# Performance work log

Hardware: AMD Instinct MI355X
Metric: run time of the kernel (lower is better)

Reference implementation:

```python
import jax, jax.numpy as jnp
import numpy as np

B, C_IN, H, W = 8, 64, 256, 256
C_OUT, K, N_KERNELS = 128, 3, 8
PAD = K // 2


def setup_inputs() -> dict:
    key = jax.random.key(0)
    k1, k2, k3, k4 = jax.random.split(key, 4)
    x = jax.random.normal(k1, (B, C_IN, H, W), dtype=jnp.float32)
    kernel_bank = jax.random.normal(k2, (N_KERNELS, C_OUT, C_IN, K, K), dtype=jnp.float32)
    # nn.Linear(in_channels, num_kernels): weight (N, C_IN), bias (N,)
    lim = 1.0 / np.sqrt(C_IN)
    attn_w = jax.random.uniform(k3, (N_KERNELS, C_IN), minval=-lim, maxval=lim, dtype=jnp.float32)
    attn_b = jax.random.uniform(k4, (N_KERNELS,), minval=-lim, maxval=lim, dtype=jnp.float32)
    return {"x": x, "kernel_bank": kernel_bank, "attn_w": attn_w, "attn_b": attn_b}


def _per_sample_conv(xi, wi):
    # xi: (C_IN, H, W), wi: (C_OUT, C_IN, K, K)
    out = jax.lax.conv_general_dilated(
        xi[None], wi, window_strides=(1, 1), padding=[(PAD, PAD), (PAD, PAD)],
        dimension_numbers=("NCHW", "OIHW", "NCHW"))
    return out[0]


def reference(x, kernel_bank, attn_w, attn_b):
    pooled = jnp.mean(x, axis=(2, 3))                      # (B, C_IN)
    logits = pooled @ attn_w.T + attn_b                     # (B, N)
    attn = jax.nn.softmax(logits, axis=1)                   # (B, N)
    # Fused kernel mix: avoid (B, N, O, I, K, K) intermediate
    mixed = jnp.einsum("bn,noihw->boihw", attn, kernel_bank)  # (B, O, I, K, K)
    return jax.vmap(_per_sample_conv)(x, mixed)             # (B, O, H, W)
```

## Files before the change

### kernel.cpp

```cpp
#include <hip/hip_runtime.h>
#include <hip/hip_bf16.h>

#define B_     8
#define C_IN   64
#define C_OUT  128
#define HW     256
#define NK     8
#define KS     3

typedef __attribute__((ext_vector_type(8))) short bf16x8;
typedef __attribute__((ext_vector_type(4))) float f32x4;

__device__ inline unsigned short f2bf(float f) {
    union { float f; unsigned int u; } a; a.f = f;
    unsigned int u = a.u;
    u += 0x7fffu + ((u >> 16) & 1u);
    return (unsigned short)(u >> 16);
}

__global__ __launch_bounds__(256) void pool_kernel(const float* __restrict__ x,
                                                   float* __restrict__ pooled) {
    const int plane = blockIdx.x;
    const float4* p = (const float4*)(x + (size_t)plane * HW * HW);
    float s = 0.f;
    for (int idx = threadIdx.x; idx < (HW * HW) / 4; idx += 256) {
        float4 v = p[idx];
        s += v.x + v.y + v.z + v.w;
    }
    #pragma unroll
    for (int off = 32; off > 0; off >>= 1) s += __shfl_down(s, off, 64);
    __shared__ float ls[4];
    const int lane = threadIdx.x & 63, wv = threadIdx.x >> 6;
    if (lane == 0) ls[wv] = s;
    __syncthreads();
    if (threadIdx.x == 0) {
        float t = ls[0] + ls[1] + ls[2] + ls[3];
        pooled[plane] = t * (1.0f / (HW * HW));
    }
}

__global__ void attn_kernel(const float* __restrict__ pooled,
                            const float* __restrict__ attn_w,
                            const float* __restrict__ attn_b,
                            float* __restrict__ attn) {
    const int t = threadIdx.x;
    const int b = t >> 3, n = t & 7;
    float s = attn_b[n];
    #pragma unroll 8
    for (int c = 0; c < C_IN; c++) s += pooled[b * C_IN + c] * attn_w[n * C_IN + c];
    __shared__ float logits[B_ * NK];
    logits[t] = s;
    __syncthreads();
    float m = -1e30f;
    #pragma unroll
    for (int j = 0; j < NK; j++) m = fmaxf(m, logits[b * NK + j]);
    float denom = 0.f;
    #pragma unroll
    for (int j = 0; j < NK; j++) denom += expf(logits[b * NK + j] - m);
    attn[t] = expf(s - m) / denom;
}

__global__ __launch_bounds__(256) void mix_kernel(const float* __restrict__ bank,
                                                  const float* __restrict__ attn,
                                                  unsigned short* __restrict__ Wt2) {
    const int PER_B = C_OUT * C_IN * KS * KS;
    int idx = blockIdx.x * 256 + threadIdx.x;
    int b = idx / PER_B;
    int r = idx % PER_B;
    float s = 0.f;
    #pragma unroll
    for (int n = 0; n < NK; n++) s += attn[b * NK + n] * bank[(size_t)n * PER_B + r];
    int kw = r % 3;
    int t1 = r / 3;
    int kh = t1 % 3;
    int t2 = t1 / 3;
    int i = t2 & 63;
    int o = t2 >> 6;
    size_t off = (((size_t)((b * 3 + kh) * 3 + kw) * 2 + (i >> 5)) * 128 + o) * 32 + (i & 31);
    Wt2[off] = f2bf(s);
}

__global__ __launch_bounds__(256) void conv_mfma(const float* __restrict__ x,
                                                 const short* __restrict__ Wt2,
                                                 float* __restrict__ out) {
    const int w0 = blockIdx.x * 128;
    const int h  = blockIdx.y;
    const int b  = blockIdx.z;

    const int t    = threadIdx.x;
    const int lane = t & 63;
    const int wid  = t >> 6;
    const int wm   = (wid & 1) * 64;
    const int wn   = (wid >> 1) * 64;
    const int l15  = lane & 15;
    const int quad = lane >> 4;

    __shared__ short sxs[130 * 72];

    f32x4 acc[4][4];
    #pragma unroll
    for (int mt = 0; mt < 4; mt++)
        #pragma unroll
        for (int nt = 0; nt < 4; nt++)
            acc[mt][nt] = (f32x4){0.f, 0.f, 0.f, 0.f};

    for (int kh = 0; kh < 3; kh++) {
        __syncthreads();
        const int hr = h + kh - 1;
        const bool rv = (hr >= 0) && (hr < HW);
        {
            const int wl = t & 127;
            const int w  = w0 + wl - 1;
            const bool wvalid = rv && (w >= 0) && (w < HW);
            #pragma unroll
            for (int it = 0; it < 16; it++) {
                const int ip = it * 2 + (t >> 7);
                float v0 = 0.f, v1 = 0.f;
                if (wvalid) {
                    const float* px = x + (((size_t)(b * C_IN + 2 * ip) * HW + hr) * HW + w);
                    v0 = px[0];
                    v1 = px[HW * HW];
                }
                ushort2 u;
                u.x = f2bf(v0);
                u.y = f2bf(v1);
                *(ushort2*)&sxs[wl * 72 + 2 * ip] = u;
            }
            if (t < 128) {
                const int i2  = t >> 1;
                const int wl2 = 128 + (t & 1);
                const int w2  = w0 + wl2 - 1;
                unsigned short uv = 0;
                if (rv && w2 < HW)
                    uv = f2bf(x[((size_t)(b * C_IN + i2) * HW + hr) * HW + w2]);
                ((unsigned short*)sxs)[wl2 * 72 + i2] = uv;
            }
        }
        __syncthreads();

        const short* wbase = Wt2 + (size_t)((b * 3 + kh) * 3) * 2 * 4096;
        #pragma unroll
        for (int kw = 0; kw < 3; kw++) {
            #pragma unroll
            for (int ic = 0; ic < 2; ic++) {
                const short* Ap = wbase + (size_t)(kw * 2 + ic) * 4096
                                + (wm + l15) * 32 + quad * 8;
                bf16x8 a0 = *(const bf16x8*)(Ap);
                bf16x8 a1 = *(const bf16x8*)(Ap + 512);
                bf16x8 a2 = *(const bf16x8*)(Ap + 1024);
                bf16x8 a3 = *(const bf16x8*)(Ap + 1536);
                const short* Bp = sxs + (wn + l15 + kw) * 72 + ic * 32 + quad * 8;
                bf16x8 b0 = *(const bf16x8*)(Bp);
                bf16x8 b1 = *(const bf16x8*)(Bp + 16 * 72);
                bf16x8 b2 = *(const bf16x8*)(Bp + 32 * 72);
                bf16x8 b3 = *(const bf16x8*)(Bp + 48 * 72);
                acc[0][0] = __builtin_amdgcn_mfma_f32_16x16x32_bf16(a0, b0, acc[0][0], 0, 0, 0);
                acc[0][1] = __builtin_amdgcn_mfma_f32_16x16x32_bf16(a0, b1, acc[0][1], 0, 0, 0);
                acc[0][2] = __builtin_amdgcn_mfma_f32_16x16x32_bf16(a0, b2, acc[0][2], 0, 0, 0);
                acc[0][3] = __builtin_amdgcn_mfma_f32_16x16x32_bf16(a0, b3, acc[0][3], 0, 0, 0);
                acc[1][0] = __builtin_amdgcn_mfma_f32_16x16x32_bf16(a1, b0, acc[1][0], 0, 0, 0);
                acc[1][1] = __builtin_amdgcn_mfma_f32_16x16x32_bf16(a1, b1, acc[1][1], 0, 0, 0);
                acc[1][2] = __builtin_amdgcn_mfma_f32_16x16x32_bf16(a1, b2, acc[1][2], 0, 0, 0);
                acc[1][3] = __builtin_amdgcn_mfma_f32_16x16x32_bf16(a1, b3, acc[1][3], 0, 0, 0);
                acc[2][0] = __builtin_amdgcn_mfma_f32_16x16x32_bf16(a2, b0, acc[2][0], 0, 0, 0);
                acc[2][1] = __builtin_amdgcn_mfma_f32_16x16x32_bf16(a2, b1, acc[2][1], 0, 0, 0);
                acc[2][2] = __builtin_amdgcn_mfma_f32_16x16x32_bf16(a2, b2, acc[2][2], 0, 0, 0);
                acc[2][3] = __builtin_amdgcn_mfma_f32_16x16x32_bf16(a2, b3, acc[2][3], 0, 0, 0);
                acc[3][0] = __builtin_amdgcn_mfma_f32_16x16x32_bf16(a3, b0, acc[3][0], 0, 0, 0);
                acc[3][1] = __builtin_amdgcn_mfma_f32_16x16x32_bf16(a3, b1, acc[3][1], 0, 0, 0);
                acc[3][2] = __builtin_amdgcn_mfma_f32_16x16x32_bf16(a3, b2, acc[3][2], 0, 0, 0);
                acc[3][3] = __builtin_amdgcn_mfma_f32_16x16x32_bf16(a3, b3, acc[3][3], 0, 0, 0);
            }
        }
    }

    #pragma unroll
    for (int mt = 0; mt < 4; mt++) {
        const int o = wm + mt * 16 + quad * 4;
        #pragma unroll
        for (int nt = 0; nt < 4; nt++) {
            const int w = w0 + wn + nt * 16 + l15;
            float* op = out + (((size_t)(b * C_OUT + o) * HW + h) * HW + w);
            #pragma unroll
            for (int r = 0; r < 4; r++) op[(size_t)r * HW * HW] = acc[mt][nt][r];
        }
    }
}

extern "C" void kernel_launch(void* const* d_in, const int* in_sizes, int n_in,
                              void* d_out, int out_size, void* d_ws, size_t ws_size,
                              hipStream_t stream) {
    const float* x      = (const float*)d_in[0];
    const float* bank   = (const float*)d_in[1];
    const float* attn_w = (const float*)d_in[2];
    const float* attn_b = (const float*)d_in[3];
    float* out = (float*)d_out;

    unsigned short* Wt2 = (unsigned short*)d_ws;
    float* pooled = (float*)((char*)d_ws + 589824 * sizeof(short));
    float* attn   = pooled + B_ * C_IN;

    pool_kernel<<<B_ * C_IN, 256, 0, stream>>>(x, pooled);
    attn_kernel<<<1, 64, 0, stream>>>(pooled, attn_w, attn_b, attn);
    mix_kernel<<<(B_ * C_OUT * C_IN * KS * KS) / 256, 256, 0, stream>>>(bank, attn, Wt2);
    conv_mfma<<<dim3(2, HW, B_), 256, 0, stream>>>(x, (const short*)Wt2, out);
}
```

Baseline: 547.1 us.

## Pre-transpose input to padded bf16 NHWC and pipeline row slabs via LDS DMA

Adds a prepass that converts x into a zero-padded, channel-innermost, XOR-swizzled bf16 layout and computes the pooled means alongside it with atomics, replacing the separate pool pass. The conv kernel now processes 8 output rows per block and streams input rows through a 4-slot LDS ring with global_load_lds, prefetching three rows ahead, so each input row is reused across its three kh taps instead of being reloaded and reconverted from fp32. The cost is an extra pass that writes about 68 MB of bf16 plus a larger workspace requirement. If the workspace is too small, the code falls back to the old path.

```diff
diff --git a/kernel.cpp b/kernel.cpp
--- a/kernel.cpp
+++ b/kernel.cpp
@@ -10,6 +10,7 @@
 
 typedef __attribute__((ext_vector_type(8))) short bf16x8;
 typedef __attribute__((ext_vector_type(4))) float f32x4;
+typedef __attribute__((ext_vector_type(4))) unsigned int u32x4;
 
 __device__ inline unsigned short f2bf(float f) {
     union { float f; unsigned int u; } a; a.f = f;
@@ -17,25 +18,68 @@
     u += 0x7fffu + ((u >> 16) & 1u);
     return (unsigned short)(u >> 16);
 }
-
-__global__ __launch_bounds__(256) void pool_kernel(const float* __restrict__ x,
-                                                   float* __restrict__ pooled) {
-    const int plane = blockIdx.x;
-    const float4* p = (const float4*)(x + (size_t)plane * HW * HW);
+__device__ inline float bf2f(unsigned short u) {
+    union { float f; unsigned int u; } a; a.u = ((unsigned int)u) << 16; return a.f;
+}
+
+#define XT_PLANE  (258 * 64)
+#define SLAB_B    16640
+
+__global__ __launch_bounds__(256) void prepass_kernel(const float* __restrict__ x,
+                                                      unsigned short* __restrict__ xT,
+                                                      float* __restrict__ pooled) {
+    const int hp = blockIdx.x;
+    const int b  = blockIdx.y;
+    const int t  = threadIdx.x;
+    unsigned short* plane = xT + ((size_t)b * 258 + hp) * XT_PLANE;
+
+    if (hp == 0 || hp == 257) {
+        f32x4 z = {0.f, 0.f, 0.f, 0.f};
+        for (int ofs = t * 16; ofs < XT_PLANE * 2; ofs += 256 * 16)
+            *(f32x4*)((char*)plane + ofs) = z;
+        return;
+    }
+    const int h = hp - 1;
+
+    __shared__ unsigned short tile[256 * 66];
+    __shared__ float psum[4][64];
+
+    const float* xp = x + ((size_t)b * C_IN * HW + h) * HW + t;
+    unsigned int pk[32];
+    #pragma unroll
+    for (int ci = 0; ci < 32; ci++) {
+        float v0 = xp[(size_t)(2 * ci) * (HW * HW)];
+        float v1 = xp[(size_t)(2 * ci + 1) * (HW * HW)];
+        unsigned int p = (unsigned int)f2bf(v0) | ((unsigned int)f2bf(v1) << 16);
+        pk[ci] = p;
+        *(unsigned int*)&tile[t * 66 + 2 * ci] = p;
+    }
+
+    unsigned short* rowp = plane + (size_t)(t + 1) * 64;
+    const int sw = (t + 1) & 7;
+    #pragma unroll
+    for (int j = 0; j < 8; j++) {
+        u32x4 v; v[0] = pk[4*j]; v[1] = pk[4*j+1]; v[2] = pk[4*j+2]; v[3] = pk[4*j+3];
+        *(u32x4*)(rowp + (size_t)((j ^ sw) * 8)) = v;
+    }
+    if (t < 2) {
+        unsigned short* zr = plane + (size_t)(t ? 257 : 0) * 64;
+        f32x4 z = {0.f, 0.f, 0.f, 0.f};
+        #pragma unroll
+        for (int j = 0; j < 8; j++) *(f32x4*)((char*)zr + j * 16) = z;
+    }
+
+    __syncthreads();
+    const int c = t & 63, part = t >> 6;
     float s = 0.f;
-    for (int idx = threadIdx.x; idx < (HW * HW) / 4; idx += 256) {
-        float4 v = p[idx];
-        s += v.x + v.y + v.z + v.w;
-    }
-    #pragma unroll
-    for (int off = 32; off > 0; off >>= 1) s += __shfl_down(s, off, 64);
-    __shared__ float ls[4];
-    const int lane = threadIdx.x & 63, wv = threadIdx.x >> 6;
-    if (lane == 0) ls[wv] = s;
+    #pragma unroll 8
+    for (int i = 0; i < 64; i++)
+        s += bf2f(tile[(part * 64 + i) * 66 + c]);
+    psum[part][c] = s;
     __syncthreads();
-    if (threadIdx.x == 0) {
-        float t = ls[0] + ls[1] + ls[2] + ls[3];
-        pooled[plane] = t * (1.0f / (HW * HW));
+    if (t < 64) {
+        float tot = (psum[0][t] + psum[1][t]) + (psum[2][t] + psum[3][t]);
+        atomicAdd(pooled + b * C_IN + t, tot * (1.0f / (HW * HW)));
     }
 }
 
@@ -80,13 +124,12 @@
     Wt2[off] = f2bf(s);
 }
 
-__global__ __launch_bounds__(256) void conv_mfma(const float* __restrict__ x,
-                                                 const short* __restrict__ Wt2,
-                                                 float* __restrict__ out) {
+__global__ __launch_bounds__(256, 2) void conv_mfma2(const unsigned short* __restrict__ xT,
+                                                     const short* __restrict__ Wt2,
+                                                     float* __restrict__ out) {
     const int w0 = blockIdx.x * 128;
-    const int h  = blockIdx.y;
+    const int h0 = blockIdx.y * 8;
     const int b  = blockIdx.z;
-
     const int t    = threadIdx.x;
     const int lane = t & 63;
     const int wid  = t >> 6;
@@ -95,15 +138,138 @@
     const int l15  = lane & 15;
     const int quad = lane >> 4;
 
+    __shared__ short sxs[4 * 8320];
+
+    #define STAGE(HP) do {                                                            \
+        const char* _src = (const char*)(xT + (((size_t)b * 258 + (size_t)(HP)) * 258 \
+                                               + (size_t)w0) * 64);                   \
+        char* _dst = (char*)sxs + (((HP) & 3) * SLAB_B);                              \
+        const int _wo = wid * 4096;                                                   \
+        __builtin_amdgcn_global_load_lds((const __attribute__((address_space(1))) void*)(_src + _wo +    lane * 16), (__attribute__((address_space(3))) void*)(_dst + _wo),        16, 0, 0); \
+        __builtin_amdgcn_global_load_lds((const __attribute__((address_space(1))) void*)(_src + _wo + 1024 + lane * 16), (__attribute__((address_space(3))) void*)(_dst + _wo + 1024), 16, 0, 0); \
+        __builtin_amdgcn_global_load_lds((const __attribute__((address_space(1))) void*)(_src + _wo + 2048 + lane * 16), (__attribute__((address_space(3))) void*)(_dst + _wo + 2048), 16, 0, 0); \
+        __builtin_amdgcn_global_load_lds((const __attribute__((address_space(1))) void*)(_src + _wo + 3072 + lane * 16), (__attribute__((address_space(3))) void*)(_dst + _wo + 3072), 16, 0, 0); \
+        __builtin_amdgcn_global_load_lds((const __attribute__((address_space(1))) void*)(_src + 16384 + lane * 4),       (__attribute__((address_space(3))) void*)(_dst + 16384),        4, 0, 0); \
+    } while (0)
+
+    const short* wt_b = Wt2 + (size_t)b * (9 * 2 * 4096);
+
+    STAGE(h0); STAGE(h0 + 1); STAGE(h0 + 2);
+
+    #pragma unroll 1
+    for (int h = h0; h < h0 + 8; ++h) {
+        __builtin_amdgcn_s_barrier();
+        if (h <= h0 + 6) {
+            STAGE(h + 3);
+            asm volatile("s_waitcnt vmcnt(5)" ::: "memory");
+        } else {
+            asm volatile("s_waitcnt vmcnt(0)" ::: "memory");
+        }
+        __builtin_amdgcn_s_barrier();
+
+        f32x4 acc[4][4];
+        #pragma unroll
+        for (int mt = 0; mt < 4; mt++)
+            #pragma unroll
+            for (int nt = 0; nt < 4; nt++)
+                acc[mt][nt] = (f32x4){0.f, 0.f, 0.f, 0.f};
+
+        #pragma unroll
+        for (int kh = 0; kh < 3; kh++) {
+            const short* buf = sxs + ((h + kh) & 3) * 8320;
+            const short* wbase = wt_b + kh * (3 * 2 * 4096);
+            #pragma unroll
+            for (int kw = 0; kw < 3; kw++) {
+                const int row = wn + l15 + kw;
+                const int rx  = row & 7;
+                #pragma unroll
+                for (int ic = 0; ic < 2; ic++) {
+                    const short* Ap = wbase + (kw * 2 + ic) * 4096 + (wm + l15) * 32 + quad * 8;
+                    bf16x8 a0 = *(const bf16x8*)(Ap);
+                    bf16x8 a1 = *(const bf16x8*)(Ap + 512);
+                    bf16x8 a2 = *(const bf16x8*)(Ap + 1024);
+                    bf16x8 a3 = *(const bf16x8*)(Ap + 1536);
+                    const short* Bp = buf + row * 64 + (((ic << 2) + quad) ^ rx) * 8;
+                    bf16x8 b0 = *(const bf16x8*)(Bp);
+                    bf16x8 b1 = *(const bf16x8*)(Bp + 1024);
+                    bf16x8 b2 = *(const bf16x8*)(Bp + 2048);
+                    bf16x8 b3 = *(const bf16x8*)(Bp + 3072);
+                    acc[0][0] = __builtin_amdgcn_mfma_f32_16x16x32_bf16(a0, b0, acc[0][0], 0, 0, 0);
+                    acc[0][1] = __builtin_amdgcn_mfma_f32_16x16x32_bf16(a0, b1, acc[0][1], 0, 0, 0);
+                    acc[0][2] = __builtin_amdgcn_mfma_f32_16x16x32_bf16(a0, b2, acc[0][2], 0, 0, 0);
+                    acc[0][3] = __builtin_amdgcn_mfma_f32_16x16x32_bf16(a0, b3, acc[0][3], 0, 0, 0);
+                    acc[1][0] = __builtin_amdgcn_mfma_f32_16x16x32_bf16(a1, b0, acc[1][0], 0, 0, 0);
+                    acc[1][1] = __builtin_amdgcn_mfma_f32_16x16x32_bf16(a1, b1, acc[1][1], 0, 0, 0);
+                    acc[1][2] = __builtin_amdgcn_mfma_f32_16x16x32_bf16(a1, b2, acc[1][2], 0, 0, 0);
+                    acc[1][3] = __builtin_amdgcn_mfma_f32_16x16x32_bf16(a1, b3, acc[1][3], 0, 0, 0);
+                    acc[2][0] = __builtin_amdgcn_mfma_f32_16x16x32_bf16(a2, b0, acc[2][0], 0, 0, 0);
+                    acc[2][1] = __builtin_amdgcn_mfma_f32_16x16x32_bf16(a2, b1, acc[2][1], 0, 0, 0);
+                    acc[2][2] = __builtin_amdgcn_mfma_f32_16x16x32_bf16(a2, b2, acc[2][2], 0, 0, 0);
+                    acc[2][3] = __builtin_amdgcn_mfma_f32_16x16x32_bf16(a2, b3, acc[2][3], 0, 0, 0);
+                    acc[3][0] = __builtin_amdgcn_mfma_f32_16x16x32_bf16(a3, b0, acc[3][0], 0, 0, 0);
+                    acc[3][1] = __builtin_amdgcn_mfma_f32_16x16x32_bf16(a3, b1, acc[3][1], 0, 0, 0);
+                    acc[3][2] = __builtin_amdgcn_mfma_f32_16x16x32_bf16(a3, b2, acc[3][2], 0, 0, 0);
+                    acc[3][3] = __builtin_amdgcn_mfma_f32_16x16x32_bf16(a3, b3, acc[3][3], 0, 0, 0);
+                }
+            }
+        }
+
+        #pragma unroll
+        for (int mt = 0; mt < 4; mt++) {
+            const int o = wm + mt * 16 + quad * 4;
+            #pragma unroll
+            for (int nt = 0; nt < 4; nt++) {
+                const int w = w0 + wn + nt * 16 + l15;
+                float* op = out + (((size_t)(b * C_OUT + o) * HW + h) * HW + w);
+                #pragma unroll
+                for (int r = 0; r < 4; r++) op[(size_t)r * HW * HW] = acc[mt][nt][r];
+            }
+        }
+    }
+    #undef STAGE
+}
+
+__global__ __launch_bounds__(256) void pool_kernel(const float* __restrict__ x,
+                                                   float* __restrict__ pooled) {
+    const int plane = blockIdx.x;
+    const float4* p = (const float4*)(x + (size_t)plane * HW * HW);
+    float s = 0.f;
+    for (int idx = threadIdx.x; idx < (HW * HW) / 4; idx += 256) {
+        float4 v = p[idx];
+        s += v.x + v.y + v.z + v.w;
+    }
+    #pragma unroll
+    for (int off = 32; off > 0; off >>= 1) s += __shfl_down(s, off, 64);
+    __shared__ float ls[4];
+    const int lane = threadIdx.x & 63, wv = threadIdx.x >> 6;
+    if (lane == 0) ls[wv] = s;
+    __syncthreads();
+    if (threadIdx.x == 0) {
+        float t = ls[0] + ls[1] + ls[2] + ls[3];
+        pooled[plane] = t * (1.0f / (HW * HW));
+    }
+}
+
+__global__ __launch_bounds__(256) void conv_mfma(const float* __restrict__ x,
+                                                 const short* __restrict__ Wt2,
+                                                 float* __restrict__ out) {
+    const int w0 = blockIdx.x * 128;
+    const int h  = blockIdx.y;
+    const int b  = blockIdx.z;
+    const int t    = threadIdx.x;
+    const int lane = t & 63;
+    const int wid  = t >> 6;
+    const int wm   = (wid & 1) * 64;
+    const int wn   = (wid >> 1) * 64;
+    const int l15  = lane & 15;
+    const int quad = lane >> 4;
     __shared__ short sxs[130 * 72];
-
     f32x4 acc[4][4];
     #pragma unroll
     for (int mt = 0; mt < 4; mt++)
         #pragma unroll
         for (int nt = 0; nt < 4; nt++)
             acc[mt][nt] = (f32x4){0.f, 0.f, 0.f, 0.f};
-
     for (int kh = 0; kh < 3; kh++) {
         __syncthreads();
         const int hr = h + kh - 1;
@@ -137,7 +303,6 @@
             }
         }
         __syncthreads();
-
         const short* wbase = Wt2 + (size_t)((b * 3 + kh) * 3) * 2 * 4096;
         #pragma unroll
         for (int kw = 0; kw < 3; kw++) {
@@ -173,7 +338,6 @@
             }
         }
     }
-
     #pragma unroll
     for (int mt = 0; mt < 4; mt++) {
         const int o = wm + mt * 16 + quad * 4;
@@ -196,12 +360,28 @@
     const float* attn_b = (const float*)d_in[3];
     float* out = (float*)d_out;
 
-    unsigned short* Wt2 = (unsigned short*)d_ws;
-    float* pooled = (float*)((char*)d_ws + 589824 * sizeof(short));
-    float* attn   = pooled + B_ * C_IN;
-
-    pool_kernel<<<B_ * C_IN, 256, 0, stream>>>(x, pooled);
-    attn_kernel<<<1, 64, 0, stream>>>(pooled, attn_w, attn_b, attn);
-    mix_kernel<<<(B_ * C_OUT * C_IN * KS * KS) / 256, 256, 0, stream>>>(bank, attn, Wt2);
-    conv_mfma<<<dim3(2, HW, B_), 256, 0, stream>>>(x, (const short*)Wt2, out);
-}
+    const size_t XT_BYTES  = (size_t)B_ * 258 * XT_PLANE * sizeof(short);
+    const size_t WT2_BYTES = (size_t)B_ * C_OUT * C_IN * KS * KS * sizeof(short);
+    const size_t NEED = XT_BYTES + WT2_BYTES + (size_t)(B_ * C_IN + B_ * NK) * 4 + 256;
+
+    if (ws_size >= NEED) {
+        unsigned short* xT  = (unsigned short*)d_ws;
+        unsigned short* Wt2 = (unsigned short*)((char*)d_ws + XT_BYTES);
+        float* pooled = (float*)((char*)d_ws + XT_BYTES + WT2_BYTES);
+        float* attn   = pooled + B_ * C_IN;
+
+        hipMemsetAsync(pooled, 0, B_ * C_IN * sizeof(float), stream);
+        prepass_kernel<<<dim3(258, B_), 256, 0, stream>>>(x, xT, pooled);
+        attn_kernel<<<1, 64, 0, stream>>>(pooled, attn_w, attn_b, attn);
+        mix_kernel<<<(B_ * C_OUT * C_IN * KS * KS) / 256, 256, 0, stream>>>(bank, attn, Wt2);
+        conv_mfma2<<<dim3(2, HW / 8, B_), 256, 0, stream>>>(xT, (const short*)Wt2, out);
+    } else {
+        unsigned short* Wt2 = (unsigned short*)d_ws;
+        float* pooled = (float*)((char*)d_ws + 589824 * sizeof(short));
+        float* attn   = pooled + B_ * C_IN;
+        pool_kernel<<<B_ * C_IN, 256, 0, stream>>>(x, pooled);
+        attn_kernel<<<1, 64, 0, stream>>>(pooled, attn_w, attn_b, attn);
+        mix_kernel<<<(B_ * C_OUT * C_IN * KS * KS) / 256, 256, 0, stream>>>(bank, attn, Wt2);
+        conv_mfma<<<dim3(2, HW, B_), 256, 0, stream>>>(x, (const short*)Wt2, out);
+    }
+}
```

After: 478.3 us. -12.6%, faster.
